# Performance work log

Measured on AMD Instinct MI355X. Metric: run time of the kernel, lower is better.

Reference implementation:

```python
import jax, jax.numpy as jnp
import numpy as np

B, S, E = 4, 2048, 1024

def setup_inputs() -> dict:
    key = jax.random.key(0)
    ks = jax.random.split(key, 6)
    values = jax.random.normal(ks[0], (B, S, E), dtype=jnp.float32)
    keys_t = jax.random.normal(ks[1], (B, S, E), dtype=jnp.float32)
    query = jax.random.normal(ks[2], (B, S, E), dtype=jnp.float32)
    mask = jax.random.randint(ks[3], (B, 1, S), 0, 2, dtype=jnp.int32)
    W_out = jax.random.normal(ks[4], (E, E), dtype=jnp.float32) * (1.0 / np.sqrt(E))
    b_out = jax.random.normal(ks[5], (E,), dtype=jnp.float32) * 0.01
    return {"values": values, "keys": keys_t, "query": query, "mask": mask,
            "W_out": W_out, "b_out": b_out}

def reference(values, keys, query, mask, W_out, b_out):
    # scores: [B, S, S] = Q K^T / sqrt(embed_size)  (NOTE: module scales by
    # sqrt(embed_size), not sqrt(head_dim), and never applies q/k/v Linears)
    scale = 1.0 / jnp.sqrt(jnp.asarray(E, dtype=query.dtype))
    scores = jnp.einsum('bqe,bke->bqk', query, keys) * scale
    scores = jnp.where(mask == 0, -jnp.inf, scores)  # masked_fill(mask==0, -inf)
    attn = jax.nn.softmax(scores, axis=-1)
    out = jnp.einsum('bqk,bke->bqe', attn, values)
    # fc_out: torch Linear -> x @ W^T + b
    return out @ W_out.T + b_out
```

## Files before the change

### kernel.cpp

```cpp
#include <hip/hip_runtime.h>

#define BB 4
#define SS 2048
#define EE 1024

typedef _Float16 f16;
typedef _Float16 f16x4 __attribute__((ext_vector_type(4)));
typedef _Float16 f16x8 __attribute__((ext_vector_type(8)));
typedef float f32x4 __attribute__((ext_vector_type(4)));

typedef const __attribute__((address_space(1))) void* gas_ptr;
typedef __attribute__((address_space(3))) void* las_ptr;

__device__ __forceinline__ void gl_lds16(const void* g, void* l) {
  __builtin_amdgcn_global_load_lds((gas_ptr)g, (las_ptr)l, 16, 0, 0);
}

#define BAR() __builtin_amdgcn_s_barrier()
#define PRIO1() __builtin_amdgcn_s_setprio(1)
#define PRIO0() __builtin_amdgcn_s_setprio(0)
#define WAITV6() asm volatile("s_waitcnt vmcnt(6)" ::: "memory")
#define WAITV0() asm volatile("s_waitcnt vmcnt(0)" ::: "memory")

__global__ __launch_bounds__(256) void prep(const int* __restrict__ mask,
                                            int* __restrict__ pos,
                                            int2* __restrict__ cnt,
                                            f16* __restrict__ Kc,
                                            f16* __restrict__ Vc) {
  const int b = blockIdx.x, t = threadIdx.x;
  const int* mb = mask + b * SS;
  int4 a0 = ((const int4*)mb)[t * 2];
  int4 a1 = ((const int4*)mb)[t * 2 + 1];
  int m[8] = {a0.x, a0.y, a0.z, a0.w, a1.x, a1.y, a1.z, a1.w};
  int tot = 0;
#pragma unroll
  for (int j = 0; j < 8; ++j) tot += m[j];
  __shared__ int sc[256];
  sc[t] = tot;
  __syncthreads();
  for (int off = 1; off < 256; off <<= 1) {
    int v = (t >= off) ? sc[t - off] : 0;
    __syncthreads();
    sc[t] += v;
    __syncthreads();
  }
  const int count = sc[255];
  const int padded = (count + 127) & ~127;
  int run = sc[t] - tot;
#pragma unroll
  for (int j = 0; j < 8; ++j) {
    pos[b * SS + t * 8 + j] = run;
    run += m[j];
  }
  if (t == 0) cnt[b] = make_int2(count, padded);
  const int nz = (padded - count) * 128;
  f16x8 z = {};
  for (int i = t; i < nz; i += 256) {
    int r = count + (i >> 7), cc = i & 127;
    ((f16x8*)(Kc + ((long)b * SS + r) * EE))[cc] = z;
    ((f16x8*)(Vc + ((long)b * SS + r) * EE))[cc] = z;
  }
}

__global__ __launch_bounds__(256) void prep2(const float* __restrict__ Q,
                                             const float* __restrict__ W,
                                             const float* __restrict__ K,
                                             const float* __restrict__ V,
                                             const int* __restrict__ mask,
                                             const int* __restrict__ pos,
                                             const int2* __restrict__ cnt,
                                             f16* __restrict__ Qh,
                                             f16* __restrict__ Wh,
                                             f16* __restrict__ Kc,
                                             f16* __restrict__ Vc,
                                             float* __restrict__ rowsum,
                                             int* __restrict__ items,
                                             int* __restrict__ nit) {
  const int x = blockIdx.x, t = threadIdx.x;
  if (x < 4608) {
    const float* in = (x < 4096) ? Q : W;
    f16* out = (x < 4096) ? Qh : Wh;
    long i = (long)(x < 4096 ? x : x - 4096) * 256 + t;
    float4 v0 = ((const float4*)in)[i * 2];
    float4 v1 = ((const float4*)in)[i * 2 + 1];
    f16x8 o;
    o[0] = (f16)v0.x; o[1] = (f16)v0.y; o[2] = (f16)v0.z; o[3] = (f16)v0.w;
    o[4] = (f16)v1.x; o[5] = (f16)v1.y; o[6] = (f16)v1.z; o[7] = (f16)v1.w;
    ((f16x8*)out)[i] = o;
    return;
  }
  if (x == 4608) {
    float4 z = {0.f, 0.f, 0.f, 0.f};
#pragma unroll
    for (int r = 0; r < 8; ++r) ((float4*)rowsum)[t + r * 256] = z;
    return;
  }
  if (x == 4609) {
    if (t < 48) {
      int nbx[4], pre[5];
      pre[0] = 0;
#pragma unroll
      for (int z = 0; z < 4; ++z) {
        nbx[z] = cnt[z].y >> 7;
        pre[z + 1] = pre[z] + nbx[z];
      }
      if (t < 32) {
        int bz = t >> 3, by = t & 7;
        int base = 8 * pre[bz] + by * nbx[bz];
        for (int bx = 0; bx < nbx[bz]; ++bx)
          items[base + bx] = bx | (by << 8) | (bz << 16);
      } else {
        int p = t - 32, bz = p >> 2, by = p & 3;
        int base = 8 * pre[4] + 4 * pre[bz] + by * nbx[bz];
        for (int bx = 0; bx < nbx[bz]; ++bx)
          items[base + bx] = bx | (by << 8) | (bz << 16) | (1 << 24);
      }
      if (t == 0) nit[0] = 12 * pre[4];
    }
    return;
  }
  const int r = x - 4610, b = r >> 11, s = r & (SS - 1);
  if (!mask[b * SS + s]) return;
  const int p = pos[b * SS + s];
  float4 kv = ((const float4*)(K + ((long)b * SS + s) * EE))[t];
  float4 vv = ((const float4*)(V + ((long)b * SS + s) * EE))[t];
  f16x4 ko, vo;
  ko[0] = (f16)kv.x; ko[1] = (f16)kv.y; ko[2] = (f16)kv.z; ko[3] = (f16)kv.w;
  vo[0] = (f16)vv.x; vo[1] = (f16)vv.y; vo[2] = (f16)vv.z; vo[3] = (f16)vv.w;
  ((f16x4*)(Kc + ((long)b * SS + p) * EE))[t] = ko;
  ((f16x4*)(Vc + ((long)b * SS + p) * EE))[t] = vo;
}

__device__ __forceinline__ void stage64(const f16* g, long K, f16* l, int h, int t) {
  int rr = t >> 3, sp = t & 7;
  int row = h * 64 + rr;
  int sl = sp ^ (rr & 7);
  gl_lds16(g + (long)row * K + (sl << 3), (char*)l + ((row << 6) + (sp << 3)) * 2);
}

__device__ __forceinline__ void read_a(f16x8 (&d)[4][2], const f16* base, int q,
                                       int wm, int l15, int l4) {
#pragma unroll
  for (int mf = 0; mf < 4; ++mf)
#pragma unroll
    for (int kk = 0; kk < 2; ++kk) {
      int row = wm * 128 + (q * 4 + mf) * 16 + l15;
      int sl = kk * 4 + l4;
      d[mf][kk] = *(const f16x8*)(base + row * 64 + ((sl ^ (row & 7)) << 3));
    }
}

__device__ __forceinline__ void read_b1(f16x8 (&d)[2], const f16* base, int f,
                                        int wn, int l15, int l4) {
#pragma unroll
  for (int kk = 0; kk < 2; ++kk) {
    int row = wn * 32 + f * 16 + l15;
    int sl = kk * 4 + l4;
    d[kk] = *(const f16x8*)(base + row * 64 + ((sl ^ (row & 7)) << 3));
  }
}

__device__ __forceinline__ void mfma_n(f32x4 (&acc)[8][2], const f16x8 (&Af)[4][2],
                                       const f16x8 (&Bf)[2], int q, int f) {
#pragma unroll
  for (int mf = 0; mf < 4; ++mf)
#pragma unroll
    for (int kk = 0; kk < 2; ++kk)
      acc[q * 4 + mf][f] = __builtin_amdgcn_mfma_f32_16x16x32_f16(
          Af[mf][kk], Bf[kk], acc[q * 4 + mf][f], 0, 0, 0);
}

__device__ __forceinline__ void n128_core(f32x4 (&acc)[8][2], const f16* Ag,
                                          const f16* Bg, long L, int NT,
                                          f16* lds, int tid, int wm, int wn,
                                          int l15, int l4) {
  f16* As0 = lds;
  f16* As1 = lds + 16384;
  f16* Bs0 = lds + 32768;
  f16* Bs1 = lds + 40960;
  f16x8 a[4][2], b[2], b2[2];
  const int NIT = NT >> 1;

  stage64(Bg, L, Bs0, 0, tid); stage64(Bg, L, Bs0, 1, tid);
#pragma unroll
  for (int h = 0; h < 4; ++h) stage64(Ag, L, As0, h, tid);
  stage64(Bg + 64, L, Bs1, 0, tid); stage64(Bg + 64, L, Bs1, 1, tid);
#pragma unroll
  for (int h = 0; h < 4; ++h) stage64(Ag + 64, L, As1, h, tid);
  WAITV6();
  BAR();

  for (int i = 0; i < NIT; ++i) {
    int t2 = 2 * i + 2, t3 = 2 * i + 3;
    long k2 = (long)((t2 < NT) ? t2 : NT - 1) << 6;
    long k3 = (long)((t3 < NT) ? t3 : NT - 1) << 6;
    read_a(a, As0, 0, wm, l15, l4);
    read_b1(b, Bs0, 0, wn, l15, l4);
    BAR(); PRIO1(); mfma_n(acc, a, b, 0, 0); PRIO0(); BAR();
    read_b1(b2, Bs0, 1, wn, l15, l4);
    BAR(); PRIO1(); mfma_n(acc, a, b2, 0, 1); PRIO0(); BAR();
    read_a(a, As0, 1, wm, l15, l4);
    stage64(Bg + k2, L, Bs0, 0, tid); stage64(Bg + k2, L, Bs0, 1, tid);
    BAR(); PRIO1(); mfma_n(acc, a, b2, 1, 1); PRIO0(); BAR();
#pragma unroll
    for (int h = 0; h < 4; ++h) stage64(Ag + k2, L, As0, h, tid);
    BAR(); PRIO1(); mfma_n(acc, a, b, 1, 0); PRIO0();
    WAITV6();
    BAR();
    read_a(a, As1, 0, wm, l15, l4);
    read_b1(b, Bs1, 0, wn, l15, l4);
    BAR(); PRIO1(); mfma_n(acc, a, b, 0, 0); PRIO0(); BAR();
    read_b1(b2, Bs1, 1, wn, l15, l4);
    BAR(); PRIO1(); mfma_n(acc, a, b2, 0, 1); PRIO0(); BAR();
    read_a(a, As1, 1, wm, l15, l4);
    stage64(Bg + k3, L, Bs1, 0, tid); stage64(Bg + k3, L, Bs1, 1, tid);
    BAR(); PRIO1(); mfma_n(acc, a, b2, 1, 1); PRIO0(); BAR();
#pragma unroll
    for (int h = 0; h < 4; ++h) stage64(Ag + k3, L, As1, h, tid);
    BAR(); PRIO1(); mfma_n(acc, a, b, 1, 0); PRIO0();
    WAITV6();
    BAR();
  }
  WAITV0();
}

__global__ __launch_bounds__(512, 1) void uber(const f16* __restrict__ Qh,
                                               const f16* __restrict__ Kc,
                                               const f16* __restrict__ Vc,
                                               const f16* __restrict__ Wh,
                                               f16* __restrict__ P,
                                               f16* __restrict__ VWt,
                                               float* __restrict__ rowsum,
                                               const int2* __restrict__ cnt,
                                               const int* __restrict__ items,
                                               const int* __restrict__ nit) {
  extern __shared__ f16 lds[];
  const int tid = threadIdx.x;
  const int lane = tid & 63, wv = tid >> 6;
  const int wm = wv >> 2, wn = wv & 3;
  const int l15 = lane & 15, l4 = lane >> 4;
  const int n = nit[0];

  for (int idx = blockIdx.x; idx < n; idx += 256) {
    const int it = items[idx];
    const int bx = it & 255, by = (it >> 8) & 255, bz = (it >> 16) & 255;
    const int kind = it >> 24;
    const long m0 = (long)by * 256;
    const long n0 = (long)bx * 128;
    const f16* Ag = kind ? (Wh + m0 * EE) : (Qh + (long)bz * SS * EE + m0 * EE);
    const f16* Bg = (kind ? Vc : Kc) + (long)bz * SS * EE + n0 * EE;

    f32x4 acc[8][2] = {};
    n128_core(acc, Ag, Bg, EE, EE >> 6, lds, tid, wm, wn, l15, l4);

    const long crow = m0 + wm * 128 + l4 * 4;
    const long ccol = n0 + wn * 32 + l15;
    if (kind == 0) {
      const int count = cnt[bz].x;
      f16* Co = P + (long)bz * SS * SS;
      float* rs = rowsum + (bz << 11);
      const float scale = 1.0f / 32.0f;
      int mv[2];
#pragma unroll
      for (int nf = 0; nf < 2; ++nf) mv[nf] = (ccol + nf * 16) < count;
#pragma unroll
      for (int mf = 0; mf < 8; ++mf)
#pragma unroll
        for (int jj = 0; jj < 4; ++jj) {
          float rp = 0.f;
#pragma unroll
          for (int nf = 0; nf < 2; ++nf) {
            float p = mv[nf] ? __expf(acc[mf][nf][jj] * scale) : 0.f;
            Co[(crow + mf * 16 + jj) * SS + ccol + nf * 16] = (f16)p;
            rp += p;
          }
          rp += __shfl_xor(rp, 1); rp += __shfl_xor(rp, 2);
          rp += __shfl_xor(rp, 4); rp += __shfl_xor(rp, 8);
          if (l15 == 0) atomicAdd(&rs[crow + mf * 16 + jj], rp);
        }
    } else {
      f16* Co = VWt + (long)bz * EE * SS;
#pragma unroll
      for (int mf = 0; mf < 8; ++mf)
#pragma unroll
        for (int nf = 0; nf < 2; ++nf)
#pragma unroll
          for (int jj = 0; jj < 4; ++jj)
            Co[(crow + mf * 16 + jj) * SS + ccol + nf * 16] = (f16)acc[mf][nf][jj];
    }
  }
}

__global__ __launch_bounds__(512, 1) void pv128(const f16* __restrict__ P,
                                                const f16* __restrict__ VWt,
                                                float* __restrict__ out,
                                                const float* __restrict__ bias,
                                                const float* __restrict__ rowsum,
                                                const int2* __restrict__ cnt) {
  extern __shared__ f16 lds[];
  int d = blockIdx.x + blockIdx.y * 8 + blockIdx.z * 64;
  int c = d & 7, j = d >> 3;
  const int bx = j & 7, by = c, bz = j >> 3;
  int2 cc = cnt[bz];
  const int padded = cc.y;
  if (padded <= 0) return;
  const long m0 = (long)by * 256;
  const long n0 = (long)bx * 128;
  const int tid = threadIdx.x;
  const int lane = tid & 63, wv = tid >> 6;
  const int wm = wv >> 2, wn = wv & 3;
  const int l15 = lane & 15, l4 = lane >> 4;
  const f16* Ag = P + (long)bz * SS * SS + m0 * SS;
  const f16* Bg = VWt + (long)bz * EE * SS + n0 * SS;

  f32x4 acc[8][2] = {};
  n128_core(acc, Ag, Bg, SS, padded >> 6, lds, tid, wm, wn, l15, l4);

  const long crow = m0 + wm * 128 + l4 * 4;
  const long ccol = n0 + wn * 32 + l15;
  float* Co = out + (long)bz * SS * EE;
  const float* rs = rowsum + (bz << 11);
  float bv[2];
#pragma unroll
  for (int nf = 0; nf < 2; ++nf) bv[nf] = bias[ccol + nf * 16];
#pragma unroll
  for (int mf = 0; mf < 8; ++mf)
#pragma unroll
    for (int jj = 0; jj < 4; ++jj) {
      float inv = 1.f / rs[crow + mf * 16 + jj];
#pragma unroll
      for (int nf = 0; nf < 2; ++nf)
        Co[(crow + mf * 16 + jj) * EE + ccol + nf * 16] =
            acc[mf][nf][jj] * inv + bv[nf];
    }
}

extern "C" void kernel_launch(void* const* d_in, const int* in_sizes, int n_in,
                              void* d_out, int out_size, void* d_ws, size_t ws_size,
                              hipStream_t stream) {
  const float* V = (const float*)d_in[0];
  const float* Kin = (const float*)d_in[1];
  const float* Q = (const float*)d_in[2];
  const int* mask = (const int*)d_in[3];
  const float* W = (const float*)d_in[4];
  const float* bias = (const float*)d_in[5];
  float* out = (float*)d_out;

  const long NE = (long)BB * SS * EE;
  f16* Qh = (f16*)d_ws;
  f16* Kc = Qh + NE;
  f16* Vc = Kc + NE;
  f16* Wh = Vc + NE;
  f16* VWt = Wh + (long)EE * EE;
  f16* P = VWt + NE;
  float* rowsum = (float*)(P + (long)BB * SS * SS);
  int* pos = (int*)(rowsum + (long)BB * SS);
  int2* cnt = (int2*)(pos + (long)BB * SS);
  int* items = (int*)(cnt + BB);
  int* nit = items + 1024;

  const size_t LDS_N = 98304;
  hipFuncSetAttribute((const void*)uber, hipFuncAttributeMaxDynamicSharedMemorySize, LDS_N);
  hipFuncSetAttribute((const void*)pv128, hipFuncAttributeMaxDynamicSharedMemorySize, LDS_N);

  prep<<<BB, 256, 0, stream>>>(mask, pos, cnt, Kc, Vc);
  prep2<<<4610 + BB * SS, 256, 0, stream>>>(Q, W, Kin, V, mask, pos, cnt,
                                            Qh, Wh, Kc, Vc, rowsum, items, nit);

  uber<<<256, 512, LDS_N, stream>>>(Qh, Kc, Vc, Wh, P, VWt, rowsum, cnt, items, nit);

  pv128<<<dim3(8, 8, BB), 512, LDS_N, stream>>>(P, VWt, out, bias, rowsum, cnt);
}
```

Baseline: 109.1 us.

## Fuse PV GEMM into persistent uber kernel with per-tile dependency counters

Removes the separate pv128 launch and adds PV work items (kind 2) to the persistent uber kernel's queue. Items are interleaved per block slot, with padding no-op items. PV tiles spin-wait on atomic counters that QK and WV tiles increment after a threadfence. This aims to cut the launch gap and the tail idle time between the two GEMM phases. In exchange it adds spin-wait and fence overhead, and it risks deadlock if item order and residency are not guaranteed.

```diff
diff --git a/kernel.cpp b/kernel.cpp
--- a/kernel.cpp
+++ b/kernel.cpp
@@ -75,7 +75,8 @@
                                              f16* __restrict__ Vc,
                                              float* __restrict__ rowsum,
                                              int* __restrict__ items,
-                                             int* __restrict__ nit) {
+                                             int* __restrict__ nit,
+                                             int* __restrict__ done) {
   const int x = blockIdx.x, t = threadIdx.x;
   if (x < 4608) {
     const float* in = (x < 4096) ? Q : W;
@@ -93,29 +94,31 @@
     float4 z = {0.f, 0.f, 0.f, 0.f};
 #pragma unroll
     for (int r = 0; r < 8; ++r) ((float4*)rowsum)[t + r * 256] = z;
+    if (t < 48) done[t] = 0;
     return;
   }
   if (x == 4609) {
-    if (t < 48) {
-      int nbx[4], pre[5];
-      pre[0] = 0;
-#pragma unroll
-      for (int z = 0; z < 4; ++z) {
-        nbx[z] = cnt[z].y >> 7;
-        pre[z + 1] = pre[z] + nbx[z];
+    if (t < 8) {
+      int nbx[4];
+#pragma unroll
+      for (int zz = 0; zz < 4; ++zz) nbx[zz] = cnt[zz].y >> 7;
+      const int sq = nbx[0] + nbx[1] + nbx[2] + nbx[3];
+      const int p02 = nbx[0] + nbx[2], p13 = nbx[1] + nbx[3];
+      const int mx = sq + (p02 > p13 ? p02 : p13) + 32;
+      int g = 0;
+      for (int zz = 0; zz < 4; ++zz)
+        for (int bx = 0; bx < nbx[zz]; ++bx)
+          items[(g++ << 3) | t] = bx | (t << 8) | (zz << 16);
+      for (int h = 0; h < 2; ++h) {
+        int zz = (t >> 2) + 2 * h;
+        for (int bx = 0; bx < nbx[zz]; ++bx)
+          items[(g++ << 3) | t] = bx | ((t & 3) << 8) | (zz << 16) | (1 << 24);
       }
-      if (t < 32) {
-        int bz = t >> 3, by = t & 7;
-        int base = 8 * pre[bz] + by * nbx[bz];
-        for (int bx = 0; bx < nbx[bz]; ++bx)
-          items[base + bx] = bx | (by << 8) | (bz << 16);
-      } else {
-        int p = t - 32, bz = p >> 2, by = p & 3;
-        int base = 8 * pre[4] + 4 * pre[bz] + by * nbx[bz];
-        for (int bx = 0; bx < nbx[bz]; ++bx)
-          items[base + bx] = bx | (by << 8) | (bz << 16) | (1 << 24);
-      }
-      if (t == 0) nit[0] = 12 * pre[4];
+      for (int zz = 0; zz < 4; ++zz)
+        for (int be = 0; be < 8; ++be)
+          items[(g++ << 3) | t] = be | (t << 8) | (zz << 16) | (2 << 24);
+      for (; g < mx; ++g) items[(g << 3) | t] = (3 << 24);
+      if (t == 0) nit[0] = mx << 3;
     }
     return;
   }
@@ -230,33 +233,63 @@
                                                const f16* __restrict__ Wh,
                                                f16* __restrict__ P,
                                                f16* __restrict__ VWt,
+                                               float* __restrict__ out,
+                                               const float* __restrict__ bias,
                                                float* __restrict__ rowsum,
                                                const int2* __restrict__ cnt,
                                                const int* __restrict__ items,
-                                               const int* __restrict__ nit) {
+                                               const int* __restrict__ nit,
+                                               int* __restrict__ done) {
   extern __shared__ f16 lds[];
   const int tid = threadIdx.x;
   const int lane = tid & 63, wv = tid >> 6;
   const int wm = wv >> 2, wn = wv & 3;
   const int l15 = lane & 15, l4 = lane >> 4;
   const int n = nit[0];
+  int* doneQK = done;
+  int* doneWV = done + 32;
 
   for (int idx = blockIdx.x; idx < n; idx += 256) {
     const int it = items[idx];
+    const int kind = (it >> 24) & 3;
+    if (kind == 3) continue;
     const int bx = it & 255, by = (it >> 8) & 255, bz = (it >> 16) & 255;
-    const int kind = it >> 24;
+    const int2 cc = cnt[bz];
     const long m0 = (long)by * 256;
     const long n0 = (long)bx * 128;
-    const f16* Ag = kind ? (Wh + m0 * EE) : (Qh + (long)bz * SS * EE + m0 * EE);
-    const f16* Bg = (kind ? Vc : Kc) + (long)bz * SS * EE + n0 * EE;
+    const f16* Ag;
+    const f16* Bg;
+    long L;
+    int NT;
+    if (kind == 0) {
+      Ag = Qh + (long)bz * SS * EE + m0 * EE; Bg = Kc + (long)bz * SS * EE + n0 * EE;
+      L = EE; NT = EE >> 6;
+    } else if (kind == 1) {
+      Ag = Wh + m0 * EE; Bg = Vc + (long)bz * SS * EE + n0 * EE;
+      L = EE; NT = EE >> 6;
+    } else {
+      const int need = cc.y >> 7;
+      if (tid == 0) {
+        while (__hip_atomic_load(&doneQK[bz * 8 + by], __ATOMIC_RELAXED,
+                                 __HIP_MEMORY_SCOPE_AGENT) < need)
+          __builtin_amdgcn_s_sleep(8);
+        while (__hip_atomic_load(&doneWV[bz * 4 + (bx >> 1)], __ATOMIC_RELAXED,
+                                 __HIP_MEMORY_SCOPE_AGENT) < need)
+          __builtin_amdgcn_s_sleep(8);
+      }
+      BAR();
+      __threadfence();
+      Ag = P + (long)bz * SS * SS + m0 * SS; Bg = VWt + (long)bz * EE * SS + n0 * SS;
+      L = SS; NT = cc.y >> 6;
+    }
 
     f32x4 acc[8][2] = {};
-    n128_core(acc, Ag, Bg, EE, EE >> 6, lds, tid, wm, wn, l15, l4);
+    n128_core(acc, Ag, Bg, L, NT, lds, tid, wm, wn, l15, l4);
 
     const long crow = m0 + wm * 128 + l4 * 4;
     const long ccol = n0 + wn * 32 + l15;
     if (kind == 0) {
-      const int count = cnt[bz].x;
+      const int count = cc.x;
       f16* Co = P + (long)bz * SS * SS;
       float* rs = rowsum + (bz << 11);
       const float scale = 1.0f / 32.0f;
@@ -278,7 +311,10 @@
           rp += __shfl_xor(rp, 4); rp += __shfl_xor(rp, 8);
           if (l15 == 0) atomicAdd(&rs[crow + mf * 16 + jj], rp);
         }
-    } else {
+      __threadfence();
+      BAR();
+      if (tid == 0) atomicAdd(&doneQK[bz * 8 + by], 1);
+    } else if (kind == 1) {
       f16* Co = VWt + (long)bz * EE * SS;
 #pragma unroll
       for (int mf = 0; mf < 8; ++mf)
@@ -287,52 +323,27 @@
 #pragma unroll
           for (int jj = 0; jj < 4; ++jj)
             Co[(crow + mf * 16 + jj) * SS + ccol + nf * 16] = (f16)acc[mf][nf][jj];
+      __threadfence();
+      BAR();
+      if (tid == 0) atomicAdd(&doneWV[bz * 4 + by], 1);
+    } else {
+      float* Co = out + (long)bz * SS * EE;
+      const float* rs = rowsum + (bz << 11);
+      float bv[2];
+#pragma unroll
+      for (int nf = 0; nf < 2; ++nf) bv[nf] = bias[ccol + nf * 16];
+#pragma unroll
+      for (int mf = 0; mf < 8; ++mf)
+#pragma unroll
+        for (int jj = 0; jj < 4; ++jj) {
+          float inv = 1.f / rs[crow + mf * 16 + jj];
+#pragma unroll
+          for (int nf = 0; nf < 2; ++nf)
+            Co[(crow + mf * 16 + jj) * EE + ccol + nf * 16] =
+                acc[mf][nf][jj] * inv + bv[nf];
+        }
     }
   }
-}
-
-__global__ __launch_bounds__(512, 1) void pv128(const f16* __restrict__ P,
-                                                const f16* __restrict__ VWt,
-                                                float* __restrict__ out,
-                                                const float* __restrict__ bias,
-                                                const float* __restrict__ rowsum,
-                                                const int2* __restrict__ cnt) {
-  extern __shared__ f16 lds[];
-  int d = blockIdx.x + blockIdx.y * 8 + blockIdx.z * 64;
-  int c = d & 7, j = d >> 3;
-  const int bx = j & 7, by = c, bz = j >> 3;
-  int2 cc = cnt[bz];
-  const int padded = cc.y;
-  if (padded <= 0) return;
-  const long m0 = (long)by * 256;
-  const long n0 = (long)bx * 128;
-  const int tid = threadIdx.x;
-  const int lane = tid & 63, wv = tid >> 6;
-  const int wm = wv >> 2, wn = wv & 3;
-  const int l15 = lane & 15, l4 = lane >> 4;
-  const f16* Ag = P + (long)bz * SS * SS + m0 * SS;
-  const f16* Bg = VWt + (long)bz * EE * SS + n0 * SS;
-
-  f32x4 acc[8][2] = {};
-  n128_core(acc, Ag, Bg, SS, padded >> 6, lds, tid, wm, wn, l15, l4);
-
-  const long crow = m0 + wm * 128 + l4 * 4;
-  const long ccol = n0 + wn * 32 + l15;
-  float* Co = out + (long)bz * SS * EE;
-  const float* rs = rowsum + (bz << 11);
-  float bv[2];
-#pragma unroll
-  for (int nf = 0; nf < 2; ++nf) bv[nf] = bias[ccol + nf * 16];
-#pragma unroll
-  for (int mf = 0; mf < 8; ++mf)
-#pragma unroll
-    for (int jj = 0; jj < 4; ++jj) {
-      float inv = 1.f / rs[crow + mf * 16 + jj];
-#pragma unroll
-      for (int nf = 0; nf < 2; ++nf)
-        Co[(crow + mf * 16 + jj) * EE + ccol + nf * 16] =
-            acc[mf][nf][jj] * inv + bv[nf];
-    }
 }
 
 extern "C" void kernel_launch(void* const* d_in, const int* in_sizes, int n_in,
@@ -358,16 +369,14 @@
   int2* cnt = (int2*)(pos + (long)BB * SS);
   int* items = (int*)(cnt + BB);
   int* nit = items + 1024;
+  int* done = nit + 1;
 
   const size_t LDS_N = 98304;
   hipFuncSetAttribute((const void*)uber, hipFuncAttributeMaxDynamicSharedMemorySize, LDS_N);
-  hipFuncSetAttribute((const void*)pv128, hipFuncAttributeMaxDynamicSharedMemorySize, LDS_N);
 
   prep<<<BB, 256, 0, stream>>>(mask, pos, cnt, Kc, Vc);
   prep2<<<4610 + BB * SS, 256, 0, stream>>>(Q, W, Kin, V, mask, pos, cnt,
-                                            Qh, Wh, Kc, Vc, rowsum, items, nit);
-
-  uber<<<256, 512, LDS_N, stream>>>(Qh, Kc, Vc, Wh, P, VWt, rowsum, cnt, items, nit);
-
-  pv128<<<dim3(8, 8, BB), 512, LDS_N, stream>>>(P, VWt, out, bias, rowsum, cnt);
-}
+                                            Qh, Wh, Kc, Vc, rowsum, items, nit, done);
+  uber<<<256, 512, LDS_N, stream>>>(Qh, Kc, Vc, Wh, P, VWt, out, bias, rowsum,
+                                    cnt, items, nit, done);
+}
```

Measured after the change: 263.6 us. 2.42x slower.
